# Kernel optimization log

Measured on AMD Instinct MI355X. Metric: run time of the kernel, lower is better.

Reference implementation:

```python
import jax, jax.numpy as jnp
import numpy as np


def setup_inputs() -> dict:
    key = jax.random.key(0)
    ks = jax.random.split(key, 7)
    B, T, C, H = 4, 4096, 1024, 64
    x = jax.random.normal(ks[0], (B, T, C), dtype=jnp.float32)
    Wq = jax.random.normal(ks[1], (C, H), dtype=jnp.float32) * 0.02
    bq = jax.random.normal(ks[2], (H,), dtype=jnp.float32) * 0.02
    Wk = jax.random.normal(ks[3], (C, H), dtype=jnp.float32) * 0.02
    bk = jax.random.normal(ks[4], (H,), dtype=jnp.float32) * 0.02
    Wv = jax.random.normal(ks[5], (C, H), dtype=jnp.float32) * 0.02
    bv = jax.random.normal(ks[6], (H,), dtype=jnp.float32) * 0.02
    return {"x": x, "Wq": Wq, "bq": bq, "Wk": Wk, "bk": bk, "Wv": Wv, "bv": bv}


def reference(x, Wq, bq, Wk, bk, Wv, bv):
    B, T, C = x.shape
    q = x @ Wq + bq            # [B,T,H]
    k = x @ Wk + bk            # [B,T,H]
    v = x @ Wv + bv            # [B,T,H]
    # NOTE: original scales by C**-0.5 where C = n_embd (input dim), not head_size
    scale = jnp.asarray(C, x.dtype) ** -0.5
    wei = jnp.einsum('bth,bsh->bts', q, k) * scale   # [B,T,T]
    causal = jnp.tril(jnp.ones((T, T), dtype=bool))
    wei = jnp.where(causal, wei, -jnp.inf)
    wei = jax.nn.softmax(wei, axis=-1)
    out = jnp.einsum('bts,bsh->bth', wei, v)         # [B,T,H]
    return out
```

## Files before the change

kernel.cpp:

```cpp
#include <hip/hip_runtime.h>
#include <hip/hip_bf16.h>

#define T_DIM 4096
#define C_DIM 1024
#define H_DIM 64
#define B_DIM 4

typedef __attribute__((ext_vector_type(8))) short short8v;
typedef __attribute__((ext_vector_type(4))) short short4v;
typedef __attribute__((ext_vector_type(4))) float float4v;

__device__ __forceinline__ unsigned short f2bf(float f) {
    __hip_bfloat16 h = __float2bfloat16(f);
    return *reinterpret_cast<unsigned short*>(&h);
}
__device__ __forceinline__ float bf2f(unsigned short u) {
    __hip_bfloat16 h = *reinterpret_cast<__hip_bfloat16*>(&u);
    return __bfloat162float(h);
}

__device__ __forceinline__ int vperm(int t5) {
    return ((t5 & 12) << 1) | (t5 & 3) | ((t5 & 16) >> 2);
}

__device__ __forceinline__ int chunk_prefix(int t) {
    const int g = t >> 3;
    return t + 4 * g * (g - 1) + (t & 7) * g;
}

#define GLL16(gsrc, ldst)                                                         \
    __builtin_amdgcn_global_load_lds(                                             \
        (const __attribute__((address_space(1))) unsigned int*)(gsrc),            \
        (__attribute__((address_space(3))) unsigned int*)(ldst), 16, 0, 0)

__global__ __launch_bounds__(256) void wprep(
    const float* __restrict__ Wq, const float* __restrict__ Wk,
    const float* __restrict__ Wv, unsigned short* __restrict__ wt)
{
    __shared__ float tile[64][65];
    const int t  = threadIdx.x;
    const int m  = blockIdx.x >> 4;
    const int k0 = (blockIdx.x & 15) * 64;
    const float* __restrict__ W = (m == 0) ? Wq : (m == 1) ? Wk : Wv;

    const int kr = t >> 4, c4 = (t & 15) * 4;
#pragma unroll
    for (int j = 0; j < 4; ++j) {
        const int row = kr + j * 16;
        const float4 v = *(const float4*)(W + (size_t)(k0 + row) * 64 + c4);
        tile[row][c4 + 0] = v.x; tile[row][c4 + 1] = v.y;
        tile[row][c4 + 2] = v.z; tile[row][c4 + 3] = v.w;
    }
    __syncthreads();

    const int col = t >> 2, q = t & 3;
    short8v s0, s1;
#pragma unroll
    for (int j = 0; j < 8; ++j) s0[j] = (short)f2bf(tile[q * 16 + j][col]);
#pragma unroll
    for (int j = 0; j < 8; ++j) s1[j] = (short)f2bf(tile[q * 16 + 8 + j][col]);
    unsigned short* dst = wt + (size_t)(m * 64 + col) * 1024 + k0 + q * 16;
    *(short8v*)dst = s0;
    *(short8v*)(dst + 8) = s1;
}

__global__ __launch_bounds__(512, 2) void qkv_gemm(
    const float* __restrict__ x, const unsigned short* __restrict__ wt,
    const float* __restrict__ bq, const float* __restrict__ bk,
    const float* __restrict__ bv,
    unsigned short* __restrict__ qb, unsigned short* __restrict__ kmat,
    unsigned short* __restrict__ vP)
{
    __shared__ __align__(16) unsigned char lx[2][4096];
    __shared__ __align__(16) unsigned char lw[3][24576];

    const int t    = threadIdx.x;
    const int lane = t & 63;
    const int w    = t >> 6;
    const int l15  = lane & 15;
    const int g4   = lane >> 4;
    const int r0   = blockIdx.x * 32;

    const int rg  = w & 1;
    const int cgr = (w >> 1) & 1;
    const int kh  = w >> 2;

    const int srow  = t >> 4;
    const int sq    = t & 15;
    const int xbyte = srow * 128 + ((sq >> 1) ^ (srow & 7)) * 16 + (sq & 1) * 8;
    const float* __restrict__ xsrc = x + (size_t)(r0 + srow) * C_DIM + sq * 4;
    const int wgs = (t & 7) ^ ((t >> 3) & 7);
    const unsigned char* __restrict__ wB = (const unsigned char*)wt;

    float4v acc[6];
#pragma unroll
    for (int cg = 0; cg < 6; ++cg) acc[cg] = (float4v){0.f, 0.f, 0.f, 0.f};

#define WSTAGE(p, kb)                                                             \
    {                                                                             \
        _Pragma("unroll")                                                         \
        for (int i = 0; i < 3; ++i)                                               \
            GLL16(wB + (size_t)(i * 64 + (t >> 3)) * 2048 + (kb) * 128 + wgs * 16,\
                  &lw[p][(i * 512 + t) * 16]);                                    \
    }
#define XCVT_WRITE(p, v)                                                          \
    {                                                                             \
        __hip_bfloat162 c0_ = __float22bfloat162_rn(make_float2((v).x, (v).y));   \
        __hip_bfloat162 c1_ = __float22bfloat162_rn(make_float2((v).z, (v).w));   \
        unsigned int* d_ = (unsigned int*)&lx[p][xbyte];                          \
        d_[0] = *(unsigned int*)&c0_;                                             \
        d_[1] = *(unsigned int*)&c1_;                                             \
    }

    float4 xvA, xvB;

    {
        const float4 x0 = *(const float4*)xsrc;
        WSTAGE(0, 0);
        WSTAGE(1, 1);
        xvA = *(const float4*)(xsrc + 64);
        XCVT_WRITE(0, x0);
        asm volatile("s_waitcnt vmcnt(4) lgkmcnt(0)" ::: "memory");
        __builtin_amdgcn_s_barrier();
    }

    const int arow = rg * 16 + l15;
    const int axor = arow & 7;
    const int kg   = kh * 4 + g4;

#pragma unroll
    for (int kb = 0; kb < 14; ++kb) {
        const int p  = kb % 3;
        const int ps = (kb + 2) % 3;
        WSTAGE(ps, kb + 2);
        if ((kb & 1) == 0) xvB = *(const float4*)(xsrc + (kb + 2) * 64);
        else               xvA = *(const float4*)(xsrc + (kb + 2) * 64);

        const short8v af = *(const short8v*)&lx[kb & 1][arow * 128 + (kg ^ axor) * 16];
#pragma unroll
        for (int cg = 0; cg < 6; ++cg) {
            const int col = cgr * 96 + cg * 16 + l15;
            const short8v bf =
                *(const short8v*)&lw[p][col * 128 + ((kg ^ (col & 7))) * 16];
            acc[cg] = __builtin_amdgcn_mfma_f32_16x16x32_bf16(af, bf, acc[cg], 0, 0, 0);
        }

        if ((kb & 1) == 0) { XCVT_WRITE((kb + 1) & 1, xvA); }
        else               { XCVT_WRITE((kb + 1) & 1, xvB); }

        asm volatile("s_waitcnt vmcnt(4) lgkmcnt(0)" ::: "memory");
        __builtin_amdgcn_s_barrier();
    }
    {
        const short8v af = *(const short8v*)&lx[0][arow * 128 + (kg ^ axor) * 16];
#pragma unroll
        for (int cg = 0; cg < 6; ++cg) {
            const int col = cgr * 96 + cg * 16 + l15;
            const short8v bf =
                *(const short8v*)&lw[2][col * 128 + ((kg ^ (col & 7))) * 16];
            acc[cg] = __builtin_amdgcn_mfma_f32_16x16x32_bf16(af, bf, acc[cg], 0, 0, 0);
        }
        XCVT_WRITE(1, xvA);
        asm volatile("s_waitcnt vmcnt(0) lgkmcnt(0)" ::: "memory");
        __builtin_amdgcn_s_barrier();
    }
    {
        const short8v af = *(const short8v*)&lx[1][arow * 128 + (kg ^ axor) * 16];
#pragma unroll
        for (int cg = 0; cg < 6; ++cg) {
            const int col = cgr * 96 + cg * 16 + l15;
            const short8v bf =
                *(const short8v*)&lw[0][col * 128 + ((kg ^ (col & 7))) * 16];
            acc[cg] = __builtin_amdgcn_mfma_f32_16x16x32_bf16(af, bf, acc[cg], 0, 0, 0);
        }
    }
    __syncthreads();

    float* comm = (float*)lw;
    if (kh == 1) {
        const int base = ((w - 4) * 64 + lane) * 24;
#pragma unroll
        for (int cg = 0; cg < 6; ++cg)
#pragma unroll
            for (int e = 0; e < 4; ++e) comm[base + cg * 4 + e] = acc[cg][e];
    }
    __syncthreads();
    if (kh == 0) {
        const int base = (w * 64 + lane) * 24;
#pragma unroll
        for (int cg = 0; cg < 6; ++cg)
#pragma unroll
            for (int e = 0; e < 4; ++e) acc[cg][e] += comm[base + cg * 4 + e];

        const float qs = 0.03125f * 1.44269504088896f;
#pragma unroll
        for (int cg = 0; cg < 6; ++cg) {
            const int cabs = cgr * 96 + cg * 16 + l15;
            const int m    = cabs >> 6;
            const int h    = cabs & 63;
            const float bb = ((m == 0) ? bq : (m == 1) ? bk : bv)[h];
#pragma unroll
            for (int rr = 0; rr < 4; ++rr) {
                const int row = r0 + rg * 16 + 4 * g4 + rr;
                const float vv = acc[cg][rr] + bb;
                if (m == 0) {
                    qb[(size_t)row * 64 + h] = f2bf(vv * qs);
                } else if (m == 1) {
                    kmat[(size_t)row * 64 + h] = f2bf(vv);
                } else {
                    const int b_i = row >> 12;
                    const int tt  = row & 4095;
                    const int tp  = (tt & ~31) | vperm(tt & 31);
                    vP[((size_t)b_i * 64 + h) * T_DIM + tp] = f2bf(vv);
                }
            }
        }
    }
#undef WSTAGE
#undef XCVT_WRITE
}

__global__ __launch_bounds__(256, 6) void attn_part(
    const unsigned short* __restrict__ qb, const unsigned short* __restrict__ kmat,
    const unsigned short* __restrict__ vP, unsigned short* __restrict__ pO,
    float* __restrict__ pl)
{
    __shared__ __align__(16) unsigned char lk[3][4096];
    __shared__ __align__(16) unsigned char lv[3][4096];

    const int tid  = threadIdx.x;
    const int w    = tid >> 6;
    const int lane = tid & 63;
    const int l15  = lane & 15;
    const int g    = lane >> 4;

    const int b   = blockIdx.x & 3;
    const int idx = 287 - (blockIdx.x >> 2);
    int t = 0;
    for (int tt = 1; tt < 64; ++tt)
        if (chunk_prefix(tt) <= idx) t = tt;
    const int c    = idx - chunk_prefix(t);
    const int q0   = t * 64;
    const int kv_l = q0 + 64;
    const int d0   = c * 512;
    const int dend = (d0 + 512 < kv_l) ? (d0 + 512) : kv_l;
    const int ns   = (dend - d0) >> 5;
    const int slot = b * 288 + idx;

    const unsigned char* kB = (const unsigned char*)kmat + (size_t)b * T_DIM * 128;
    const unsigned char* vB = (const unsigned char*)vP + (size_t)b * 64 * T_DIM * 2;
    const int krow = tid >> 3, kdg = tid & 7;
    const int vh = tid >> 2, vdg = tid & 3;
    const unsigned char* ksrc = kB + krow * 128 + ((kdg ^ (krow & 7)) * 16);
    const unsigned char* vsrc = vB + (size_t)vh * 8192 + ((vdg ^ (vh & 3)) * 16);
    const int kdst = tid * 16;

#define STAGE(p, ss)                                                          \
    {                                                                         \
        const int off_ = d0 + (ss) * 32;                                      \
        GLL16(ksrc + (size_t)off_ * 128, &lk[p][kdst]);                       \
        GLL16(vsrc + (size_t)off_ * 2,   &lv[p][kdst]);                       \
    }

    const unsigned short* qrow = qb + ((size_t)b * T_DIM + q0 + 16 * w + l15) * 64;
    const short8v qf0 = *(const short8v*)(qrow + 8 * g);
    const short8v qf1 = *(const short8v*)(qrow + 32 + 8 * g);

    short8v kones;
#pragma unroll
    for (int j = 0; j < 8; ++j) kones[j] = (short)0x3F80;

    float4v acc[4];
    float4v accl = (float4v){0.f, 0.f, 0.f, 0.f};
#pragma unroll
    for (int f = 0; f < 4; ++f) acc[f] = (float4v){0.f, 0.f, 0.f, 0.f};

    const int qmax = q0 + 16 * w + 15;
    const int kxor = l15 & 7;
    const int vxor = l15 & 3;

    STAGE(0, 0);
    STAGE(1, (ns > 1) ? 1 : 0);
    asm volatile("s_waitcnt vmcnt(2)" ::: "memory");
    __builtin_amdgcn_s_barrier();

    int p = 0;
    for (int s = 0; s < ns; ++s) {
        const int ps = (p + 2 >= 3) ? (p - 1) : (p + 2);
        const int sn = (s + 2 < ns) ? (s + 2) : (ns - 1);
        STAGE(ps, sn);

        const int kv0 = d0 + s * 32;
        if (kv0 <= qmax) {
            const short8v ka0 = *(const short8v*)&lk[p][(l15 * 8 + (g ^ kxor)) * 16];
            const short8v ka1 = *(const short8v*)&lk[p][(l15 * 8 + ((4 + g) ^ kxor)) * 16];
            const short8v ka2 = *(const short8v*)&lk[p][((16 + l15) * 8 + (g ^ kxor)) * 16];
            const short8v ka3 = *(const short8v*)&lk[p][((16 + l15) * 8 + ((4 + g) ^ kxor)) * 16];
            short8v vb[4];
#pragma unroll
            for (int f = 0; f < 4; ++f)
                vb[f] = *(const short8v*)&lv[p][((f * 16 + l15) * 4 + (g ^ vxor)) * 16];

            const float4v z = (float4v){0.f, 0.f, 0.f, 0.f};
            float4v slo = __builtin_amdgcn_mfma_f32_16x16x32_bf16(ka0, qf0, z, 0, 0, 0);
            slo = __builtin_amdgcn_mfma_f32_16x16x32_bf16(ka1, qf1, slo, 0, 0, 0);
            float4v shi = __builtin_amdgcn_mfma_f32_16x16x32_bf16(ka2, qf0, z, 0, 0, 0);
            shi = __builtin_amdgcn_mfma_f32_16x16x32_bf16(ka3, qf1, shi, 0, 0, 0);

            float pl_[4], ph_[4];
            if (kv0 + 31 <= q0 + 16 * w) {
#pragma unroll
                for (int r = 0; r < 4; ++r) {
                    pl_[r] = exp2f(slo[r]);
                    ph_[r] = exp2f(shi[r]);
                }
            } else {
                const int qabs = q0 + 16 * w + l15;
#pragma unroll
                for (int r = 0; r < 4; ++r) {
                    const int kvlo = kv0 + 4 * g + r;
                    pl_[r] = (kvlo <= qabs) ? exp2f(slo[r]) : 0.f;
                    ph_[r] = (kvlo + 16 <= qabs) ? exp2f(shi[r]) : 0.f;
                }
            }
            short8v pa;
            {
                unsigned int* pu = (unsigned int*)&pa;
                __hip_bfloat162 c0 = __float22bfloat162_rn(make_float2(pl_[0], pl_[1]));
                __hip_bfloat162 c1 = __float22bfloat162_rn(make_float2(pl_[2], pl_[3]));
                __hip_bfloat162 c2 = __float22bfloat162_rn(make_float2(ph_[0], ph_[1]));
                __hip_bfloat162 c3 = __float22bfloat162_rn(make_float2(ph_[2], ph_[3]));
                pu[0] = *(unsigned int*)&c0;
                pu[1] = *(unsigned int*)&c1;
                pu[2] = *(unsigned int*)&c2;
                pu[3] = *(unsigned int*)&c3;
            }
#pragma unroll
            for (int f = 0; f < 4; ++f)
                acc[f] = __builtin_amdgcn_mfma_f32_16x16x32_bf16(pa, vb[f], acc[f], 0, 0, 0);
            accl = __builtin_amdgcn_mfma_f32_16x16x32_bf16(pa, kones, accl, 0, 0, 0);
        }

        asm volatile("s_waitcnt vmcnt(2) lgkmcnt(0)" ::: "memory");
        __builtin_amdgcn_s_barrier();
        p = (p + 1 >= 3) ? 0 : (p + 1);
    }

    unsigned short* po = pO + (size_t)slot * 4096 + (size_t)(16 * w) * 64;
#pragma unroll
    for (int f = 0; f < 4; ++f)
#pragma unroll
        for (int r = 0; r < 4; ++r)
            po[(4 * g + r) * 64 + f * 16 + l15] = f2bf(acc[f][r]);
    if (l15 == 0) {
#pragma unroll
        for (int r = 0; r < 4; ++r)
            pl[(size_t)slot * 64 + 16 * w + 4 * g + r] = accl[r];
    }
#undef STAGE
}

__global__ __launch_bounds__(256) void attn_comb(
    const unsigned short* __restrict__ pO, const float* __restrict__ pl,
    float* __restrict__ out)
{
    const int tid  = blockIdx.x * 256 + threadIdx.x;
    const int row  = tid >> 4;
    const int h4   = (tid & 15) * 4;
    const int b    = row >> 12;
    const int brow = row & 4095;
    const int t    = brow >> 6;
    const int rr   = brow & 63;
    const int nc   = 1 + (t >> 3);
    const int base = b * 288 + chunk_prefix(t);

    const unsigned short* src = pO + (size_t)base * 4096 + rr * 64 + h4;
    const float* lsrc = pl + (size_t)base * 64 + rr;
    float4 o = make_float4(0.f, 0.f, 0.f, 0.f);
    float l = 0.f;
    for (int c = 0; c < nc; ++c) {
        const short4v s = *(const short4v*)(src + (size_t)c * 4096);
        o.x += bf2f((unsigned short)s[0]);
        o.y += bf2f((unsigned short)s[1]);
        o.z += bf2f((unsigned short)s[2]);
        o.w += bf2f((unsigned short)s[3]);
        l += lsrc[(size_t)c * 64];
    }
    const float inv = 1.f / l;
    o.x *= inv; o.y *= inv; o.z *= inv; o.w *= inv;
    *(float4*)(out + (size_t)row * 64 + h4) = o;
}

extern "C" void kernel_launch(void* const* d_in, const int* in_sizes, int n_in,
                              void* d_out, int out_size, void* d_ws, size_t ws_size,
                              hipStream_t stream) {
    const float* x  = (const float*)d_in[0];
    const float* Wq = (const float*)d_in[1];
    const float* bq = (const float*)d_in[2];
    const float* Wk = (const float*)d_in[3];
    const float* bk = (const float*)d_in[4];
    const float* Wv = (const float*)d_in[5];
    const float* bv = (const float*)d_in[6];
    float* out = (float*)d_out;

    char* ws = (char*)d_ws;
    unsigned short* qb   = (unsigned short*)(ws);
    unsigned short* kmat = (unsigned short*)(ws + (2u << 20));
    unsigned short* vP   = (unsigned short*)(ws + (4u << 20));
    unsigned short* wt   = (unsigned short*)(ws + (6u << 20));
    unsigned short* pO   = (unsigned short*)(ws + (8u << 20));
    float*          pl   = (float*)(ws + (8u << 20) + 9437184u);

    wprep<<<48, 256, 0, stream>>>(Wq, Wk, Wv, wt);
    qkv_gemm<<<512, 512, 0, stream>>>(x, wt, bq, bk, bv, qb, kmat, vP);
    attn_part<<<1152, 256, 0, stream>>>(qb, kmat, vP, pO, pl);
    attn_comb<<<1024, 256, 0, stream>>>(pO, pl, out);
}
```

Baseline: 56.18 us.

## Read QKV weights directly from global memory with smaller 16-row GEMM blocks

The QKV projection GEMM no longer stages the transposed weight tiles through LDS with async loads. Each lane now reads its bf16 weight fragments straight from global memory, relying on cache since all blocks share the weights. Blocks shrink to 256 threads covering 16 rows, launched as 1024 blocks with a dedicated small LDS reduction buffer, which cuts LDS use and should raise occupancy. It also lowers attn_part's launch-bounds occupancy hint from 6 to 4, and the cost is exposed global-load latency per MFMA step.

```diff
diff --git a/kernel.cpp b/kernel.cpp
--- a/kernel.cpp
+++ b/kernel.cpp
@@ -64,45 +64,35 @@
     *(short8v*)(dst + 8) = s1;
 }
 
-__global__ __launch_bounds__(512, 2) void qkv_gemm(
+__global__ __launch_bounds__(256, 4) void qkv_gemm(
     const float* __restrict__ x, const unsigned short* __restrict__ wt,
     const float* __restrict__ bq, const float* __restrict__ bk,
     const float* __restrict__ bv,
     unsigned short* __restrict__ qb, unsigned short* __restrict__ kmat,
     unsigned short* __restrict__ vP)
 {
-    __shared__ __align__(16) unsigned char lx[2][4096];
-    __shared__ __align__(16) unsigned char lw[3][24576];
+    __shared__ __align__(16) unsigned char lx[2][2048];
+    __shared__ float comm[2][64][24];
 
     const int t    = threadIdx.x;
     const int lane = t & 63;
     const int w    = t >> 6;
     const int l15  = lane & 15;
     const int g4   = lane >> 4;
-    const int r0   = blockIdx.x * 32;
-
-    const int rg  = w & 1;
-    const int cgr = (w >> 1) & 1;
-    const int kh  = w >> 2;
+    const int r0   = blockIdx.x * 16;
+
+    const int kh  = w & 1;
+    const int cgr = w >> 1;
 
     const int srow  = t >> 4;
     const int sq    = t & 15;
     const int xbyte = srow * 128 + ((sq >> 1) ^ (srow & 7)) * 16 + (sq & 1) * 8;
     const float* __restrict__ xsrc = x + (size_t)(r0 + srow) * C_DIM + sq * 4;
-    const int wgs = (t & 7) ^ ((t >> 3) & 7);
-    const unsigned char* __restrict__ wB = (const unsigned char*)wt;
 
     float4v acc[6];
 #pragma unroll
     for (int cg = 0; cg < 6; ++cg) acc[cg] = (float4v){0.f, 0.f, 0.f, 0.f};
 
-#define WSTAGE(p, kb)                                                             \
-    {                                                                             \
-        _Pragma("unroll")                                                         \
-        for (int i = 0; i < 3; ++i)                                               \
-            GLL16(wB + (size_t)(i * 64 + (t >> 3)) * 2048 + (kb) * 128 + wgs * 16,\
-                  &lw[p][(i * 512 + t) * 16]);                                    \
-    }
 #define XCVT_WRITE(p, v)                                                          \
     {                                                                             \
         __hip_bfloat162 c0_ = __float22bfloat162_rn(make_float2((v).x, (v).y));   \
@@ -116,48 +106,40 @@
 
     {
         const float4 x0 = *(const float4*)xsrc;
-        WSTAGE(0, 0);
-        WSTAGE(1, 1);
         xvA = *(const float4*)(xsrc + 64);
         XCVT_WRITE(0, x0);
-        asm volatile("s_waitcnt vmcnt(4) lgkmcnt(0)" ::: "memory");
+        asm volatile("s_waitcnt vmcnt(2) lgkmcnt(0)" ::: "memory");
         __builtin_amdgcn_s_barrier();
     }
 
-    const int arow = rg * 16 + l15;
-    const int axor = arow & 7;
+    const int axor = l15 & 7;
     const int kg   = kh * 4 + g4;
-
-#pragma unroll
+    const unsigned short* __restrict__ wb0 =
+        wt + (size_t)(cgr * 96 + l15) * 1024 + kh * 32 + g4 * 8;
+
     for (int kb = 0; kb < 14; ++kb) {
-        const int p  = kb % 3;
-        const int ps = (kb + 2) % 3;
-        WSTAGE(ps, kb + 2);
+        const int p = kb & 1;
         if ((kb & 1) == 0) xvB = *(const float4*)(xsrc + (kb + 2) * 64);
         else               xvA = *(const float4*)(xsrc + (kb + 2) * 64);
 
-        const short8v af = *(const short8v*)&lx[kb & 1][arow * 128 + (kg ^ axor) * 16];
+        const short8v af = *(const short8v*)&lx[p][l15 * 128 + (kg ^ axor) * 16];
 #pragma unroll
         for (int cg = 0; cg < 6; ++cg) {
-            const int col = cgr * 96 + cg * 16 + l15;
-            const short8v bf =
-                *(const short8v*)&lw[p][col * 128 + ((kg ^ (col & 7))) * 16];
+            const short8v bf = *(const short8v*)(wb0 + (size_t)(cg * 16) * 1024 + kb * 64);
             acc[cg] = __builtin_amdgcn_mfma_f32_16x16x32_bf16(af, bf, acc[cg], 0, 0, 0);
         }
 
-        if ((kb & 1) == 0) { XCVT_WRITE((kb + 1) & 1, xvA); }
-        else               { XCVT_WRITE((kb + 1) & 1, xvB); }
-
-        asm volatile("s_waitcnt vmcnt(4) lgkmcnt(0)" ::: "memory");
+        if ((kb & 1) == 0) { XCVT_WRITE(p ^ 1, xvA); }
+        else               { XCVT_WRITE(p ^ 1, xvB); }
+
+        asm volatile("s_waitcnt vmcnt(2) lgkmcnt(0)" ::: "memory");
         __builtin_amdgcn_s_barrier();
     }
     {
-        const short8v af = *(const short8v*)&lx[0][arow * 128 + (kg ^ axor) * 16];
+        const short8v af = *(const short8v*)&lx[0][l15 * 128 + (kg ^ axor) * 16];
 #pragma unroll
         for (int cg = 0; cg < 6; ++cg) {
-            const int col = cgr * 96 + cg * 16 + l15;
-            const short8v bf =
-                *(const short8v*)&lw[2][col * 128 + ((kg ^ (col & 7))) * 16];
+            const short8v bf = *(const short8v*)(wb0 + (size_t)(cg * 16) * 1024 + 14 * 64);
             acc[cg] = __builtin_amdgcn_mfma_f32_16x16x32_bf16(af, bf, acc[cg], 0, 0, 0);
         }
         XCVT_WRITE(1, xvA);
@@ -165,32 +147,29 @@
         __builtin_amdgcn_s_barrier();
     }
     {
-        const short8v af = *(const short8v*)&lx[1][arow * 128 + (kg ^ axor) * 16];
+        const short8v af = *(const short8v*)&lx[1][l15 * 128 + (kg ^ axor) * 16];
 #pragma unroll
         for (int cg = 0; cg < 6; ++cg) {
-            const int col = cgr * 96 + cg * 16 + l15;
-            const short8v bf =
-                *(const short8v*)&lw[0][col * 128 + ((kg ^ (col & 7))) * 16];
+            const short8v bf = *(const short8v*)(wb0 + (size_t)(cg * 16) * 1024 + 15 * 64);
             acc[cg] = __builtin_amdgcn_mfma_f32_16x16x32_bf16(af, bf, acc[cg], 0, 0, 0);
         }
     }
     __syncthreads();
 
-    float* comm = (float*)lw;
     if (kh == 1) {
-        const int base = ((w - 4) * 64 + lane) * 24;
 #pragma unroll
         for (int cg = 0; cg < 6; ++cg)
 #pragma unroll
-            for (int e = 0; e < 4; ++e) comm[base + cg * 4 + e] = acc[cg][e];
+            for (int e = 0; e < 4; ++e)
+                comm[cgr][lane][cg * 4 + e] = acc[cg][e];
     }
     __syncthreads();
     if (kh == 0) {
-        const int base = (w * 64 + lane) * 24;
 #pragma unroll
         for (int cg = 0; cg < 6; ++cg)
 #pragma unroll
-            for (int e = 0; e < 4; ++e) acc[cg][e] += comm[base + cg * 4 + e];
+            for (int e = 0; e < 4; ++e)
+                acc[cg][e] += comm[cgr][lane][cg * 4 + e];
 
         const float qs = 0.03125f * 1.44269504088896f;
 #pragma unroll
@@ -201,7 +180,7 @@
             const float bb = ((m == 0) ? bq : (m == 1) ? bk : bv)[h];
 #pragma unroll
             for (int rr = 0; rr < 4; ++rr) {
-                const int row = r0 + rg * 16 + 4 * g4 + rr;
+                const int row = r0 + 4 * g4 + rr;
                 const float vv = acc[cg][rr] + bb;
                 if (m == 0) {
                     qb[(size_t)row * 64 + h] = f2bf(vv * qs);
@@ -216,11 +195,10 @@
             }
         }
     }
-#undef WSTAGE
 #undef XCVT_WRITE
 }
 
-__global__ __launch_bounds__(256, 6) void attn_part(
+__global__ __launch_bounds__(256, 4) void attn_part(
     const unsigned short* __restrict__ qb, const unsigned short* __restrict__ kmat,
     const unsigned short* __restrict__ vP, unsigned short* __restrict__ pO,
     float* __restrict__ pl)
@@ -412,7 +390,7 @@
     float*          pl   = (float*)(ws + (8u << 20) + 9437184u);
 
     wprep<<<48, 256, 0, stream>>>(Wq, Wk, Wv, wt);
-    qkv_gemm<<<512, 512, 0, stream>>>(x, wt, bq, bk, bv, qb, kmat, vP);
+    qkv_gemm<<<1024, 256, 0, stream>>>(x, wt, bq, bk, bv, qb, kmat, vP);
     attn_part<<<1152, 256, 0, stream>>>(qb, kmat, vP, pO, pl);
     attn_comb<<<1024, 256, 0, stream>>>(pO, pl, out);
 }
```

Result: slower. 86.36 us (+53.7%).
